# Kernel tuning notes

Hardware: AMD Instinct MI355X
Metric: run time of the kernel (lower is better)

## Reference

```python
import jax, jax.numpy as jnp
import numpy as np

E = 128       # embed_dim
H = 128       # hidden_dim
NLABEL = 5
VOCAB = 50000
DEPTH = 18    # levels 0..17, complete binary tree
BRANCH = 2
N_NODES = 2 ** DEPTH - 1  # level-order layout: level l occupies [2^l-1, 2^(l+1)-1)


def setup_inputs() -> dict:
    key = jax.random.key(0)
    ks = jax.random.split(key, 24)

    def w(k, shape):
        return jax.random.normal(k, shape, dtype=jnp.float32) * 0.05

    inp = {
        "embeds": w(ks[0], (VOCAB, E)),
        "node_words": jax.random.randint(ks[1], (N_NODES,), 0, VOCAB),
        "node_labels": jax.random.randint(ks[2], (N_NODES,), 0, NLABEL),
        "depth": DEPTH,
        "branching": BRANCH,
    }
    # 8 gate linears: *x maps E->H, *h maps H->H (torch nn.Linear: y = x @ W.T + b)
    for j, nm in enumerate(["ix", "ih", "fx", "fh", "ox", "oh", "ux", "uh"]):
        in_dim = E if nm.endswith("x") else H
        inp["W" + nm] = w(ks[3 + 2 * j], (H, in_dim))
        inp["b" + nm] = w(ks[4 + 2 * j], (H,))
    inp["Wout"] = w(ks[20], (NLABEL, H))
    inp["bout"] = w(ks[21], (NLABEL,))
    return inp


def _lin(x, W, b):
    return x @ W.T + b


def _tree_lstm(embeds, node_words, node_labels, depth, branching,
               Wix, bix, Wih, bih, Wfx, bfx, Wfh, bfh,
               Wox, box, Woh, boh, Wux, bux, Wuh, buh, Wout, bout):
    b = branching
    hid = Wix.shape[0]
    loss = jnp.zeros((), dtype=embeds.dtype)
    child_c = child_h = None
    logp = None
    # bottom-up over levels (leaves first); level l has b^l nodes at offset (b^l-1)/(b-1)
    for l in range(depth - 1, -1, -1):
        n = b ** l
        off = (b ** l - 1) // (b - 1)
        x = embeds[node_words[off:off + n]]            # [n, E]
        if child_h is None:                            # leaves: zero child states
            h_sum = jnp.zeros((n, hid), dtype=embeds.dtype)
            c_agg = jnp.zeros((n, hid), dtype=embeds.dtype)
        else:
            ch = child_h.reshape(n, b, hid)            # children of each level-l node
            cc = child_c.reshape(n, b, hid)
            h_sum = ch.sum(axis=1)                     # child-sum
            f = jax.nn.sigmoid(_lin(x, Wfx, bfx)[:, None, :] + _lin(ch, Wfh, bfh))
            c_agg = (f * cc).sum(axis=1)               # sum_k f_k * c_k
        i = jax.nn.sigmoid(_lin(x, Wix, bix) + _lin(h_sum, Wih, bih))
        o = jax.nn.sigmoid(_lin(x, Wox, box) + _lin(h_sum, Woh, boh))
        u = jnp.tanh(_lin(x, Wux, bux) + _lin(h_sum, Wuh, buh))
        c = i * u + c_agg
        h = o * jnp.tanh(c)
        logp = jax.nn.log_softmax(_lin(h, Wout, bout), axis=-1)   # [n, NLABEL]
        lab = node_labels[off:off + n]
        loss = loss - logp[jnp.arange(n), lab].sum()              # NLL summed over nodes
        child_c, child_h = c, h
    return logp, loss  # logp from level 0 = root log-probs [1, NLABEL]


def reference(embeds, node_words, node_labels, depth, branching,
              Wix, bix, Wih, bih, Wfx, bfx, Wfh, bfh,
              Wox, box, Woh, boh, Wux, bux, Wuh, buh, Wout, bout):
    return _tree_lstm(embeds, node_words, node_labels, depth, branching,
                      Wix, bix, Wih, bih, Wfx, bfx, Wfh, bfh,
                      Wox, box, Woh, boh, Wux, bux, Wuh, buh, Wout, bout)
```

## Files before the change

### kernel.cpp

```cpp
#include <hip/hip_runtime.h>
#include <math.h>

#define DEPTH 18
#define NINT ((1 << (DEPTH - 1)) - 1)
#define LEAF_OFF ((1 << (DEPTH - 2)) - 1)
#define NVOCAB 50000
#define SAW 520

typedef unsigned short bf16raw;
typedef __bf16 bf16x8 __attribute__((ext_vector_type(8)));
typedef float f32x4 __attribute__((ext_vector_type(4)));
typedef short short8 __attribute__((ext_vector_type(8)));

__device__ __forceinline__ float sigm(float x) { return 1.0f / (1.0f + __expf(-x)); }
__device__ __forceinline__ float fast_tanh(float x) {
    float t = __expf(2.0f * x);
    return 1.0f - 2.0f / (t + 1.0f);
}

__device__ __forceinline__ float bf2f(bf16raw u) {
    union { unsigned int i; float f; } v;
    v.i = ((unsigned int)u) << 16;
    return v.f;
}
__device__ __forceinline__ bf16raw f2bf(float f) {
    union { float f; unsigned int i; } v;
    v.f = f;
    unsigned int r = v.i + 0x7FFFu + ((v.i >> 16) & 1u);
    return (bf16raw)(r >> 16);
}

#define SB() __builtin_amdgcn_sched_barrier(0)

__global__ __launch_bounds__(256) void k_prep_embeds(const float* __restrict__ src,
                                                     bf16raw* __restrict__ dst, int n4)
{
    int i = blockIdx.x * blockDim.x + threadIdx.x;
    if (i < n4) {
        float4 v = ((const float4*)src)[i];
        ushort4 o;
        o.x = f2bf(v.x); o.y = f2bf(v.y); o.z = f2bf(v.z); o.w = f2bf(v.w);
        ((ushort4*)dst)[i] = o;
    }
}

__global__ __launch_bounds__(128) void k_prep_bcat(
    const float* __restrict__ Wix, const float* __restrict__ bix,
    const float* __restrict__ Wih, const float* __restrict__ bih,
    const float* __restrict__ Wfx, const float* __restrict__ bfx,
    const float* __restrict__ Wfh, const float* __restrict__ bfh,
    const float* __restrict__ Wox, const float* __restrict__ box_,
    const float* __restrict__ Woh, const float* __restrict__ boh,
    const float* __restrict__ Wux, const float* __restrict__ bux,
    const float* __restrict__ Wuh, const float* __restrict__ buh,
    bf16raw* __restrict__ Bfrag, float* __restrict__ bias_cat)
{
    const int j = blockIdx.x;
    const int gate = j >> 7, jj = j & 127;
    const float *Wx, *Wh, *bx, *bh;
    switch (gate) {
        case 0: Wx = Wix; Wh = Wih; bx = bix;  bh = bih; break;
        case 1: Wx = Wux; Wh = Wuh; bx = bux;  bh = buh; break;
        case 2: Wx = Wox; Wh = Woh; bx = box_; bh = boh; break;
        default: Wx = Wfx; Wh = Wfh; bx = bfx; bh = bfh; break;
    }
    const int coltile = (j >> 4) & 7, lr = j & 15;
    for (int k = threadIdx.x; k < 256; k += blockDim.x) {
        float v = (k < 128) ? Wx[jj * 128 + k] : Wh[jj * 128 + (k - 128)];
        const int idx = (((gate * 8 + coltile) * 8 + (k >> 5)) * 64
                         + ((k >> 3) & 3) * 16 + lr) * 8 + (k & 7);
        Bfrag[idx] = f2bf(v);
    }
    if (threadIdx.x == 0) bias_cat[j] = bx[jj] + bh[jj];
}

template<int CB>
__device__ __forceinline__ void lp_burst(const bf16raw* __restrict__ bfbase, int wcol,
                                         bf16x8 (&bb)[16])
{
#pragma unroll
    for (int kt = 0; kt < 4; ++kt)
#pragma unroll
        for (int j = 0; j < 4; ++j)
            bb[kt * 4 + j] = *(const bf16x8*)(bfbase +
                    (long)(((CB * 8 + (wcol >> 4) + j) * 8 + kt) * 512));
}

__device__ __forceinline__ void lp_mfma_all(const bf16raw* __restrict__ sA, int wrow,
                                            int lrow, int lquad,
                                            bf16x8 (&bb)[16], f32x4 (&acc)[4][4])
{
#pragma unroll
    for (int kt = 0; kt < 4; ++kt) {
        bf16x8 af[4];
#pragma unroll
        for (int i = 0; i < 4; ++i)
            af[i] = *(const bf16x8*)&sA[(wrow + i * 16 + lrow) * 136 + kt * 32 + lquad * 8];
#pragma unroll
        for (int i = 0; i < 4; ++i)
#pragma unroll
            for (int j = 0; j < 4; ++j)
                acc[i][j] = __builtin_amdgcn_mfma_f32_16x16x32_bf16(af[i], bb[kt * 4 + j], acc[i][j], 0, 0, 0);
    }
}

template<int CB>
__device__ __forceinline__ void lp_rungemm(const bf16raw* __restrict__ sA,
                                           const bf16raw* __restrict__ bfbase,
                                           int wrow, int wcol, int lrow, int lquad,
                                           f32x4 (&acc)[4][4])
{
#pragma unroll
    for (int i = 0; i < 4; i++)
#pragma unroll
        for (int j = 0; j < 4; j++) acc[i][j] = (f32x4){0.f, 0.f, 0.f, 0.f};
    bf16x8 bb[16];
    lp_burst<CB>(bfbase, wcol, bb);
    SB();
    lp_mfma_all(sA, wrow, lrow, lquad, bb, acc);
}

template<int G, int H>
__device__ __forceinline__ void load8(const bf16raw* __restrict__ bfbase, int w,
                                      bf16x8 (&bb)[8])
{
#pragma unroll
    for (int kt2 = 0; kt2 < 4; ++kt2)
#pragma unroll
        for (int jj = 0; jj < 2; ++jj)
            bb[kt2 * 2 + jj] = *(const bf16x8*)(bfbase +
                    (long)(((G * 8 + w * 2 + jj) * 8 + H * 4 + kt2) * 512));
}

template<int PASS, int H>
__device__ __forceinline__ void mfma8(const bf16raw* __restrict__ sA, int lrow, int lquad,
                                      bf16x8 (&bb)[8], f32x4 (&acc)[2][2])
{
    constexpr int base = (PASS == 2) ? (H ? 8 : 0)
                       : (PASS == 3) ? (H ? 12 : 0)
                       : H * 4;
#pragma unroll
    for (int kt2 = 0; kt2 < 4; ++kt2) {
        bf16x8 af[2];
#pragma unroll
        for (int i = 0; i < 2; ++i)
            af[i] = *(const bf16x8*)&sA[(i * 16 + lrow) * SAW + (base + kt2) * 32 + lquad * 8];
#pragma unroll
        for (int jj = 0; jj < 2; ++jj)
#pragma unroll
            for (int i = 0; i < 2; ++i)
                acc[i][jj] = __builtin_amdgcn_mfma_f32_16x16x32_bf16(af[i], bb[kt2 * 2 + jj], acc[i][jj], 0, 0, 0);
    }
}

__global__ __launch_bounds__(256, 2) void k_leafpre(
    const bf16raw* __restrict__ embeds_bf,
    const bf16raw* __restrict__ Bfrag, const float* __restrict__ bias_cat,
    const float* __restrict__ Wout, const float* __restrict__ bout,
    bf16raw* __restrict__ hc_leaf, float* __restrict__ lossv6, int vbase, int nv)
{
    vbase += blockIdx.x * 128;
    nv -= vbase;
    if (nv > 128) nv = 128;
    if (nv <= 0) return;

    __shared__ __align__(16) bf16raw sA[128 * 136];
    __shared__ __align__(16) bf16raw sT[128 * 136];
    __shared__ float sWout[5 * 128];

    const int t = threadIdx.x;
    for (int i = t; i < 640; i += 256) sWout[i] = Wout[i];

    {
        const int row = t >> 1;
        const int half = (t & 1) * 64;
        const int arow = (row < nv) ? row : 0;
        const bf16raw* ax = embeds_bf + (long)(vbase + arow) * 128;
#pragma unroll
        for (int s = 0; s < 8; ++s)
            *(short8*)&sA[row * 136 + half + s * 8] = *(const short8*)(ax + half + s * 8);
    }

    const int lane = t & 63;
    const int w = t >> 6;
    const int wrow = (w >> 1) * 64;
    const int wcol = (w & 1) * 64;
    const int lrow = lane & 15;
    const int lquad = lane >> 4;

    __syncthreads();

    const bf16raw* bfbase = Bfrag + (long)lane * 8;

    float tval[4][4][4];
    f32x4 acc[4][4];

    lp_rungemm<0>(sA, bfbase, wrow, wcol, lrow, lquad, acc);
#pragma unroll
    for (int i = 0; i < 4; i++)
#pragma unroll
        for (int jj = 0; jj < 4; jj++) {
            const float b = bias_cat[wcol + jj * 16 + lrow];
#pragma unroll
            for (int r = 0; r < 4; r++) tval[i][jj][r] = sigm(acc[i][jj][r] + b);
        }
    lp_rungemm<1>(sA, bfbase, wrow, wcol, lrow, lquad, acc);
#pragma unroll
    for (int i = 0; i < 4; i++)
#pragma unroll
        for (int jj = 0; jj < 4; jj++) {
            const float b = bias_cat[128 + wcol + jj * 16 + lrow];
#pragma unroll
            for (int r = 0; r < 4; r++) tval[i][jj][r] *= fast_tanh(acc[i][jj][r] + b);
        }
#pragma unroll
    for (int i = 0; i < 4; i++)
#pragma unroll
        for (int jj = 0; jj < 4; jj++)
#pragma unroll
            for (int r = 0; r < 4; r++) {
                const int m = wrow + i * 16 + lquad * 4 + r;
                const int j = wcol + jj * 16 + lrow;
                sT[m * 136 + j] = f2bf(tval[i][jj][r]);
            }
#pragma unroll
    for (int i = 0; i < 4; i++)
#pragma unroll
        for (int jj = 0; jj < 4; jj++)
#pragma unroll
            for (int r = 0; r < 4; r++) tval[i][jj][r] = fast_tanh(tval[i][jj][r]);
    __syncthreads();
#pragma unroll
    for (int s = 0; s < 8; ++s) {
        int ci = t + 256 * s;
        int row = ci >> 4, c8 = (ci & 15) * 8;
        if (row < nv)
            *(short8*)(hc_leaf + (long)(vbase + row) * 256 + 128 + c8) = *(const short8*)&sT[row * 136 + c8];
    }
    lp_rungemm<2>(sA, bfbase, wrow, wcol, lrow, lquad, acc);
    __syncthreads();
#pragma unroll
    for (int i = 0; i < 4; i++)
#pragma unroll
        for (int jj = 0; jj < 4; jj++) {
            const float b = bias_cat[256 + wcol + jj * 16 + lrow];
#pragma unroll
            for (int r = 0; r < 4; r++) {
                const int m = wrow + i * 16 + lquad * 4 + r;
                const int j = wcol + jj * 16 + lrow;
                sT[m * 136 + j] = f2bf(sigm(acc[i][jj][r] + b) * tval[i][jj][r]);
            }
        }
    __syncthreads();
#pragma unroll
    for (int s = 0; s < 8; ++s) {
        int ci = t + 256 * s;
        int row = ci >> 4, c8 = (ci & 15) * 8;
        if (row < nv)
            *(short8*)(hc_leaf + (long)(vbase + row) * 256 + c8) = *(const short8*)&sT[row * 136 + c8];
    }
    {
        const int row = t >> 1, half = t & 1;
        float p[5] = {0.f, 0.f, 0.f, 0.f, 0.f};
        const bf16raw* rp = &sT[row * 136 + half * 64];
#pragma unroll
        for (int s = 0; s < 8; ++s) {
            short8 v = *(const short8*)(rp + s * 8);
#pragma unroll
            for (int e = 0; e < 8; ++e) {
                float hv = bf2f((bf16raw)(unsigned short)v[e]);
#pragma unroll
                for (int l = 0; l < 5; l++) p[l] += hv * sWout[l * 128 + half * 64 + s * 8 + e];
            }
        }
#pragma unroll
        for (int l = 0; l < 5; l++) p[l] += __shfl_down(p[l], 1);
        if (half == 0 && row < nv) {
            float lg[5], mx = -1e30f;
#pragma unroll
            for (int l = 0; l < 5; l++) {
                lg[l] = p[l] + bout[l];
                mx = fmaxf(mx, lg[l]);
            }
            float se = 0.f;
#pragma unroll
            for (int l = 0; l < 5; l++) se += __expf(lg[l] - mx);
            float lse = __logf(se) + mx;
            float* dst = lossv6 + (long)(vbase + row) * 6;
#pragma unroll
            for (int l = 0; l < 5; l++) dst[l] = lg[l];
            dst[5] = lse;
        }
    }
}

__global__ __launch_bounds__(256, 3) void k_level32(
    const bf16raw* __restrict__ embeds_bf, const int* __restrict__ words,
    bf16raw* __restrict__ h_all, bf16raw* __restrict__ c_all,
    const bf16raw* __restrict__ hc_leaf,
    const bf16raw* __restrict__ Bfrag, const float* __restrict__ bias_cat,
    int off, int nm, int leafkids)
{
    __shared__ __align__(16) bf16raw sA[32 * SAW];
    __shared__ __align__(16) bf16raw sCT[64 * 136];

    const int t = threadIdx.x;
    const int m0 = blockIdx.x * 32;

    {
        const int row = t >> 3;
        const int co = (t & 7) * 8;
        int mm = m0 + row; if (mm >= nm) mm = nm - 1;
        const long g = (long)off + mm;
        const bf16raw* px = embeds_bf + (long)words[g] * 128;
        const bf16raw *p1, *p2;
        if (leafkids) {
            p1 = hc_leaf + (long)words[2 * g + 1] * 256;
            p2 = hc_leaf + (long)words[2 * g + 2] * 256;
        } else {
            p1 = h_all + (2 * g + 1) * 128;
            p2 = h_all + (2 * g + 2) * 128;
        }
        short8 vx0 = *(const short8*)(px + co);
        short8 vx1 = *(const short8*)(px + 64 + co);
        short8 h10 = *(const short8*)(p1 + co);
        short8 h11 = *(const short8*)(p1 + 64 + co);
        short8 h20 = *(const short8*)(p2 + co);
        short8 h21 = *(const short8*)(p2 + 64 + co);
        short8 hs0, hs1;
#pragma unroll
        for (int e = 0; e < 8; ++e) {
            hs0[e] = (short)f2bf(bf2f((bf16raw)(unsigned short)h10[e]) +
                                 bf2f((bf16raw)(unsigned short)h20[e]));
            hs1[e] = (short)f2bf(bf2f((bf16raw)(unsigned short)h11[e]) +
                                 bf2f((bf16raw)(unsigned short)h21[e]));
        }
        *(short8*)&sA[row * SAW + co]        = vx0;
        *(short8*)&sA[row * SAW + 64 + co]   = vx1;
        *(short8*)&sA[row * SAW + 128 + co]  = hs0;
        *(short8*)&sA[row * SAW + 192 + co]  = hs1;
        *(short8*)&sA[row * SAW + 256 + co]  = h10;
        *(short8*)&sA[row * SAW + 320 + co]  = h11;
        *(short8*)&sA[row * SAW + 384 + co]  = h20;
        *(short8*)&sA[row * SAW + 448 + co]  = h21;
    }
    {
        const int slot = t >> 2;
        const int cc8 = (t & 3) * 8;
        int mm = m0 + (slot >> 1); if (mm >= nm) mm = nm - 1;
        const long g = (long)off + mm;
        const long cg = 2 * g + 1 + (slot & 1);
        const bf16raw* pc = leafkids ? (hc_leaf + (long)words[cg] * 256 + 128)
                                     : (c_all + cg * 128);
#pragma unroll
        for (int s = 0; s < 4; ++s)
            *(short8*)&sCT[slot * 136 + s * 32 + cc8] = *(const short8*)(pc + s * 32 + cc8);
    }

    const int lane = t & 63;
    const int w = t >> 6;
    const int lrow = lane & 15;
    const int lquad = lane >> 4;

    float bias[4][2];
#pragma unroll
    for (int g = 0; g < 4; ++g)
#pragma unroll
        for (int jj = 0; jj < 2; ++jj)
            bias[g][jj] = bias_cat[g * 128 + w * 32 + jj * 16 + lrow];

    __syncthreads();

    const bf16raw* bfbase = Bfrag + (long)lane * 8;

    f32x4 acc[2][2];
    float si[2][2][4];
    float cc[2][2][4];
    float hh[2][2][4];
    bf16x8 bbA[8], bbB[8];

#define ZACC() { _Pragma("unroll") for (int i_ = 0; i_ < 2; ++i_) \
                 _Pragma("unroll") for (int j_ = 0; j_ < 2; ++j_) \
                     acc[i_][j_] = (f32x4){0.f, 0.f, 0.f, 0.f}; }

    load8<0, 0>(bfbase, w, bbA);
    load8<0, 1>(bfbase, w, bbB);
    SB();
    ZACC();
    mfma8<0, 0>(sA, lrow, lquad, bbA, acc); SB();
    load8<1, 0>(bfbase, w, bbA); SB();
    mfma8<0, 1>(sA, lrow, lquad, bbB, acc); SB();
    load8<1, 1>(bfbase, w, bbB); SB();
#pragma unroll
    for (int i = 0; i < 2; ++i)
#pragma unroll
        for (int jj = 0; jj < 2; ++jj)
#pragma unroll
            for (int r = 0; r < 4; ++r)
                si[i][jj][r] = sigm(acc[i][jj][r] + bias[0][jj]);
    ZACC();
    mfma8<1, 0>(sA, lrow, lquad, bbA, acc); SB();
    load8<3, 0>(bfbase, w, bbA); SB();
    mfma8<1, 1>(sA, lrow, lquad, bbB, acc); SB();
    load8<3, 1>(bfbase, w, bbB); SB();
#pragma unroll
    for (int i = 0; i < 2; ++i)
#pragma unroll
        for (int jj = 0; jj < 2; ++jj)
#pragma unroll
            for (int r = 0; r < 4; ++r)
                cc[i][jj][r] = si[i][jj][r] * fast_tanh(acc[i][jj][r] + bias[1][jj]);
    ZACC();
    mfma8<2, 0>(sA, lrow, lquad, bbA, acc);
    mfma8<2, 1>(sA, lrow, lquad, bbB, acc);
    SB();
#pragma unroll
    for (int i = 0; i < 2; ++i)
#pragma unroll
        for (int jj = 0; jj < 2; ++jj) {
            const int j = w * 32 + jj * 16 + lrow;
#pragma unroll
            for (int r = 0; r < 4; ++r) {
                const int m = i * 16 + lquad * 4 + r;
                cc[i][jj][r] += sigm(acc[i][jj][r] + bias[3][jj]) * bf2f(sCT[(2 * m) * 136 + j]);
            }
        }
    ZACC();
    mfma8<3, 0>(sA, lrow, lquad, bbA, acc);
    mfma8<3, 1>(sA, lrow, lquad, bbB, acc);
    SB();
    load8<2, 0>(bfbase, w, bbA);
    load8<2, 1>(bfbase, w, bbB);
    SB();
#pragma unroll
    for (int i = 0; i < 2; ++i)
#pragma unroll
        for (int jj = 0; jj < 2; ++jj) {
            const int j = w * 32 + jj * 16 + lrow;
#pragma unroll
            for (int r = 0; r < 4; ++r) {
                const int m = i * 16 + lquad * 4 + r;
                cc[i][jj][r] += sigm(acc[i][jj][r] + bias[3][jj]) * bf2f(sCT[(2 * m + 1) * 136 + j]);
            }
        }
    ZACC();
    mfma8<4, 0>(sA, lrow, lquad, bbA, acc);
    mfma8<4, 1>(sA, lrow, lquad, bbB, acc);
    SB();
#pragma unroll
    for (int i = 0; i < 2; ++i)
#pragma unroll
        for (int jj = 0; jj < 2; ++jj)
#pragma unroll
            for (int r = 0; r < 4; ++r)
                hh[i][jj][r] = sigm(acc[i][jj][r] + bias[2][jj]) * fast_tanh(cc[i][jj][r]);
#undef ZACC

    __syncthreads();

#pragma unroll
    for (int i = 0; i < 2; ++i)
#pragma unroll
        for (int jj = 0; jj < 2; ++jj) {
            const int j = w * 32 + jj * 16 + lrow;
#pragma unroll
            for (int r = 0; r < 4; ++r) {
                const int m = i * 16 + lquad * 4 + r;
                sCT[m * 136 + j] = f2bf(cc[i][jj][r]);
                sCT[(32 + m) * 136 + j] = f2bf(hh[i][jj][r]);
            }
        }
    __syncthreads();

#pragma unroll
    for (int q = 0; q < 4; ++q) {
        int ci = t + 256 * q;
        int row = ci >> 4;
        int c8 = (ci & 15) * 8;
        int m = row & 31;
        if (m0 + m < nm) {
            bf16raw* dst = (row < 32) ? c_all : h_all;
            *(short8*)(dst + ((long)off + m0 + m) * 128 + c8) = *(const short8*)&sCT[row * 136 + c8];
        }
    }
}

__global__ __launch_bounds__(256) void k_loss(
    const bf16raw* __restrict__ h_all, const int* __restrict__ words,
    const int* __restrict__ labels, const float* __restrict__ lossv6,
    const float* __restrict__ Wout, const float* __restrict__ bout,
    float* __restrict__ partials, float* __restrict__ out)
{
    __shared__ float sWout[640];
    __shared__ float red[128];
    const int t = threadIdx.x;
    for (int i = t; i < 640; i += 256) sWout[i] = Wout[i];

    const int row = t >> 1, half = t & 1;
    const long g = (long)blockIdx.x * 128 + row;
    const bool valid = g < NINT;
    const long gg = valid ? g : 0;
    __syncthreads();

    float p[5] = {0.f, 0.f, 0.f, 0.f, 0.f};
    const bf16raw* hp = h_all + gg * 128 + half * 64;
#pragma unroll
    for (int s = 0; s < 8; ++s) {
        short8 v = *(const short8*)(hp + s * 8);
#pragma unroll
        for (int e = 0; e < 8; ++e) {
            float hv = bf2f((bf16raw)(unsigned short)v[e]);
#pragma unroll
            for (int l = 0; l < 5; l++) p[l] += hv * sWout[l * 128 + half * 64 + s * 8 + e];
        }
    }
#pragma unroll
    for (int l = 0; l < 5; l++) p[l] += __shfl_down(p[l], 1);

    float lossNode = 0.f;
    if (half == 0 && valid) {
        float lg[5], mx = -1e30f;
#pragma unroll
        for (int l = 0; l < 5; l++) {
            lg[l] = p[l] + bout[l];
            mx = fmaxf(mx, lg[l]);
        }
        float se = 0.f;
#pragma unroll
        for (int l = 0; l < 5; l++) se += __expf(lg[l] - mx);
        float lse = __logf(se) + mx;
        lossNode = lse - lg[labels[gg]];
        if (gg >= LEAF_OFF) {
            const float* lv1 = lossv6 + (long)words[2 * gg + 1] * 6;
            const float* lv2 = lossv6 + (long)words[2 * gg + 2] * 6;
            lossNode += (lv1[5] - lv1[labels[2 * gg + 1]])
                      + (lv2[5] - lv2[labels[2 * gg + 2]]);
        }
        if (gg == 0) {
#pragma unroll
            for (int l = 0; l < 5; l++) out[l] = lg[l] - lse;
        }
    }
    if (half == 0) red[row] = lossNode;
    __syncthreads();
    if (t < 64) {
        float s = red[t] + red[t + 64];
#pragma unroll
        for (int d = 32; d > 0; d >>= 1) s += __shfl_down(s, d);
        if (t == 0) atomicAdd(&partials[blockIdx.x & 1023], s);
    }
}

__global__ __launch_bounds__(256) void k3_reduce(const float* __restrict__ partials,
                                                 float* __restrict__ out)
{
    const int t = threadIdx.x;
    float s = 0.f;
    for (int i = t; i < 1024; i += 256) s += partials[i];
#pragma unroll
    for (int d = 32; d > 0; d >>= 1) s += __shfl_down(s, d);
    __shared__ float red[4];
    if ((t & 63) == 0) red[t >> 6] = s;
    __syncthreads();
    if (t == 0) out[5] = red[0] + red[1] + red[2] + red[3];
}

extern "C" void kernel_launch(void* const* d_in, const int* in_sizes, int n_in,
                              void* d_out, int out_size, void* d_ws, size_t ws_size,
                              hipStream_t stream)
{
    const float* embeds = (const float*)d_in[0];
    const int* words = (const int*)d_in[1];
    const int* labels = (const int*)d_in[2];
    const float* Wix = (const float*)d_in[5],  *bix  = (const float*)d_in[6];
    const float* Wih = (const float*)d_in[7],  *bih  = (const float*)d_in[8];
    const float* Wfx = (const float*)d_in[9],  *bfx  = (const float*)d_in[10];
    const float* Wfh = (const float*)d_in[11], *bfh  = (const float*)d_in[12];
    const float* Wox = (const float*)d_in[13], *box_ = (const float*)d_in[14];
    const float* Woh = (const float*)d_in[15], *boh  = (const float*)d_in[16];
    const float* Wux = (const float*)d_in[17], *bux  = (const float*)d_in[18];
    const float* Wuh = (const float*)d_in[19], *buh  = (const float*)d_in[20];
    const float* Wout = (const float*)d_in[21], *bout = (const float*)d_in[22];
    float* out = (float*)d_out;

    char* ws = (char*)d_ws;
    const size_t treeElems = (size_t)NINT * 128;
    bf16raw* h_all = (bf16raw*)ws;
    bf16raw* c_all = h_all + treeElems;
    bf16raw* embeds_bf = c_all + treeElems;
    bf16raw* Bfrag = embeds_bf + (size_t)NVOCAB * 128;
    bf16raw* hc_leaf = Bfrag + 4 * 8 * 8 * 512;
    float* lossv6 = (float*)(hc_leaf + (size_t)NVOCAB * 256);
    float* bias_cat = lossv6 + (size_t)NVOCAB * 6;
    float* partials = bias_cat + 512;

    k_prep_embeds<<<(NVOCAB * 128 / 4 + 255) / 256, 256, 0, stream>>>(
        embeds, embeds_bf, NVOCAB * 128 / 4);
    k_prep_bcat<<<512, 128, 0, stream>>>(Wix, bix, Wih, bih, Wfx, bfx, Wfh, bfh,
                                         Wox, box_, Woh, boh, Wux, bux, Wuh, buh,
                                         Bfrag, bias_cat);
    hipMemsetAsync(partials, 0, 1024 * sizeof(float), stream);

    k_leafpre<<<(NVOCAB + 127) / 128, 256, 0, stream>>>(
        embeds_bf, Bfrag, bias_cat, Wout, bout, hc_leaf, lossv6, 0, NVOCAB);

    for (int l = DEPTH - 2; l >= 0; --l) {
        const int n = 1 << l;
        k_level32<<<dim3((n + 31) / 32), 256, 0, stream>>>(
            embeds_bf, words, h_all, c_all, hc_leaf, Bfrag, bias_cat,
            n - 1, n, (l == DEPTH - 2) ? 1 : 0);
    }

    k_loss<<<(NINT + 127) / 128, 256, 0, stream>>>(
        h_all, words, labels, lossv6, Wout, bout, partials, out);
    k3_reduce<<<1, 256, 0, stream>>>(partials, out);
}
```

Baseline: 378.0 us.

## Shrink leaf-precompute tiles to 64 rows and pad weight fragment stride

The vocabulary leaf-precompute kernel now handles 64 vocab rows per block instead of 128. Each wave covers 32x64 outputs, so the accumulator and activation registers are halved, LDS use drops, and launch bounds rise to 3 blocks per CU. The weight fragment layout is padded from 8 to 9 k-tiles per column tile, likely to spread global or cache access across channels. The trade-off is that every weight fragment is reloaded twice as often across blocks, and the output projection's LDS reads become scalar.

```diff
diff --git a/kernel.cpp b/kernel.cpp
--- a/kernel.cpp
+++ b/kernel.cpp
@@ -6,6 +6,7 @@
 #define LEAF_OFF ((1 << (DEPTH - 2)) - 1)
 #define NVOCAB 50000
 #define SAW 520
+#define KTS 9
 
 typedef unsigned short bf16raw;
 typedef __bf16 bf16x8 __attribute__((ext_vector_type(8)));
@@ -67,7 +68,7 @@
     const int coltile = (j >> 4) & 7, lr = j & 15;
     for (int k = threadIdx.x; k < 256; k += blockDim.x) {
         float v = (k < 128) ? Wx[jj * 128 + k] : Wh[jj * 128 + (k - 128)];
-        const int idx = (((gate * 8 + coltile) * 8 + (k >> 5)) * 64
+        const int idx = (((gate * 8 + coltile) * KTS + (k >> 5)) * 64
                          + ((k >> 3) & 3) * 16 + lr) * 8 + (k & 7);
         Bfrag[idx] = f2bf(v);
     }
@@ -83,21 +84,21 @@
 #pragma unroll
         for (int j = 0; j < 4; ++j)
             bb[kt * 4 + j] = *(const bf16x8*)(bfbase +
-                    (long)(((CB * 8 + (wcol >> 4) + j) * 8 + kt) * 512));
+                    (long)(((CB * 8 + (wcol >> 4) + j) * KTS + kt) * 512));
 }
 
 __device__ __forceinline__ void lp_mfma_all(const bf16raw* __restrict__ sA, int wrow,
                                             int lrow, int lquad,
-                                            bf16x8 (&bb)[16], f32x4 (&acc)[4][4])
+                                            bf16x8 (&bb)[16], f32x4 (&acc)[2][4])
 {
 #pragma unroll
     for (int kt = 0; kt < 4; ++kt) {
-        bf16x8 af[4];
-#pragma unroll
-        for (int i = 0; i < 4; ++i)
+        bf16x8 af[2];
+#pragma unroll
+        for (int i = 0; i < 2; ++i)
             af[i] = *(const bf16x8*)&sA[(wrow + i * 16 + lrow) * 136 + kt * 32 + lquad * 8];
 #pragma unroll
-        for (int i = 0; i < 4; ++i)
+        for (int i = 0; i < 2; ++i)
 #pragma unroll
             for (int j = 0; j < 4; ++j)
                 acc[i][j] = __builtin_amdgcn_mfma_f32_16x16x32_bf16(af[i], bb[kt * 4 + j], acc[i][j], 0, 0, 0);
@@ -108,10 +109,10 @@
 __device__ __forceinline__ void lp_rungemm(const bf16raw* __restrict__ sA,
                                            const bf16raw* __restrict__ bfbase,
                                            int wrow, int wcol, int lrow, int lquad,
-                                           f32x4 (&acc)[4][4])
-{
-#pragma unroll
-    for (int i = 0; i < 4; i++)
+                                           f32x4 (&acc)[2][4])
+{
+#pragma unroll
+    for (int i = 0; i < 2; i++)
 #pragma unroll
         for (int j = 0; j < 4; j++) acc[i][j] = (f32x4){0.f, 0.f, 0.f, 0.f};
     bf16x8 bb[16];
@@ -129,7 +130,7 @@
 #pragma unroll
         for (int jj = 0; jj < 2; ++jj)
             bb[kt2 * 2 + jj] = *(const bf16x8*)(bfbase +
-                    (long)(((G * 8 + w * 2 + jj) * 8 + H * 4 + kt2) * 512));
+                    (long)(((G * 8 + w * 2 + jj) * KTS + H * 4 + kt2) * 512));
 }
 
 template<int PASS, int H>
@@ -153,38 +154,39 @@
     }
 }
 
-__global__ __launch_bounds__(256, 2) void k_leafpre(
+__global__ __launch_bounds__(256, 3) void k_leafpre(
     const bf16raw* __restrict__ embeds_bf,
     const bf16raw* __restrict__ Bfrag, const float* __restrict__ bias_cat,
     const float* __restrict__ Wout, const float* __restrict__ bout,
-    bf16raw* __restrict__ hc_leaf, float* __restrict__ lossv6, int vbase, int nv)
-{
-    vbase += blockIdx.x * 128;
-    nv -= vbase;
-    if (nv > 128) nv = 128;
+    bf16raw* __restrict__ hc_leaf, float* __restrict__ lossv6, int nvtot)
+{
+    const int vbase = blockIdx.x * 64;
+    int nv = nvtot - vbase;
+    if (nv > 64) nv = 64;
     if (nv <= 0) return;
 
-    __shared__ __align__(16) bf16raw sA[128 * 136];
-    __shared__ __align__(16) bf16raw sT[128 * 136];
+    __shared__ __align__(16) bf16raw sA[64 * 136];
+    __shared__ __align__(16) bf16raw sT[64 * 136];
     __shared__ float sWout[5 * 128];
 
     const int t = threadIdx.x;
     for (int i = t; i < 640; i += 256) sWout[i] = Wout[i];
 
     {
-        const int row = t >> 1;
-        const int half = (t & 1) * 64;
+        const int row = t >> 2;
+        const int co = (t & 3) * 32;
         const int arow = (row < nv) ? row : 0;
         const bf16raw* ax = embeds_bf + (long)(vbase + arow) * 128;
-#pragma unroll
-        for (int s = 0; s < 8; ++s)
-            *(short8*)&sA[row * 136 + half + s * 8] = *(const short8*)(ax + half + s * 8);
+        *(short8*)&sA[row * 136 + co]      = *(const short8*)(ax + co);
+        *(short8*)&sA[row * 136 + co + 8]  = *(const short8*)(ax + co + 8);
+        *(short8*)&sA[row * 136 + co + 16] = *(const short8*)(ax + co + 16);
+        *(short8*)&sA[row * 136 + co + 24] = *(const short8*)(ax + co + 24);
     }
 
     const int lane = t & 63;
     const int w = t >> 6;
-    const int wrow = (w >> 1) * 64;
-    const int wcol = (w & 1) * 64;
+    const int wrow = (w & 1) * 32;
+    const int wcol = (w >> 1) * 64;
     const int lrow = lane & 15;
     const int lquad = lane >> 4;
 
@@ -192,12 +194,12 @@
 
     const bf16raw* bfbase = Bfrag + (long)lane * 8;
 
-    float tval[4][4][4];
-    f32x4 acc[4][4];
+    float tval[2][4][4];
+    f32x4 acc[2][4];
 
     lp_rungemm<0>(sA, bfbase, wrow, wcol, lrow, lquad, acc);
 #pragma unroll
-    for (int i = 0; i < 4; i++)
+    for (int i = 0; i < 2; i++)
 #pragma unroll
         for (int jj = 0; jj < 4; jj++) {
             const float b = bias_cat[wcol + jj * 16 + lrow];
@@ -206,7 +208,7 @@
         }
     lp_rungemm<1>(sA, bfbase, wrow, wcol, lrow, lquad, acc);
 #pragma unroll
-    for (int i = 0; i < 4; i++)
+    for (int i = 0; i < 2; i++)
 #pragma unroll
         for (int jj = 0; jj < 4; jj++) {
             const float b = bias_cat[128 + wcol + jj * 16 + lrow];
@@ -214,7 +216,7 @@
             for (int r = 0; r < 4; r++) tval[i][jj][r] *= fast_tanh(acc[i][jj][r] + b);
         }
 #pragma unroll
-    for (int i = 0; i < 4; i++)
+    for (int i = 0; i < 2; i++)
 #pragma unroll
         for (int jj = 0; jj < 4; jj++)
 #pragma unroll
@@ -224,14 +226,14 @@
                 sT[m * 136 + j] = f2bf(tval[i][jj][r]);
             }
 #pragma unroll
-    for (int i = 0; i < 4; i++)
+    for (int i = 0; i < 2; i++)
 #pragma unroll
         for (int jj = 0; jj < 4; jj++)
 #pragma unroll
             for (int r = 0; r < 4; r++) tval[i][jj][r] = fast_tanh(tval[i][jj][r]);
     __syncthreads();
 #pragma unroll
-    for (int s = 0; s < 8; ++s) {
+    for (int s = 0; s < 4; ++s) {
         int ci = t + 256 * s;
         int row = ci >> 4, c8 = (ci & 15) * 8;
         if (row < nv)
@@ -240,7 +242,7 @@
     lp_rungemm<2>(sA, bfbase, wrow, wcol, lrow, lquad, acc);
     __syncthreads();
 #pragma unroll
-    for (int i = 0; i < 4; i++)
+    for (int i = 0; i < 2; i++)
 #pragma unroll
         for (int jj = 0; jj < 4; jj++) {
             const float b = bias_cat[256 + wcol + jj * 16 + lrow];
@@ -253,29 +255,27 @@
         }
     __syncthreads();
 #pragma unroll
-    for (int s = 0; s < 8; ++s) {
+    for (int s = 0; s < 4; ++s) {
         int ci = t + 256 * s;
         int row = ci >> 4, c8 = (ci & 15) * 8;
         if (row < nv)
             *(short8*)(hc_leaf + (long)(vbase + row) * 256 + c8) = *(const short8*)&sT[row * 136 + c8];
     }
     {
-        const int row = t >> 1, half = t & 1;
+        const int row = t >> 2, q = t & 3;
         float p[5] = {0.f, 0.f, 0.f, 0.f, 0.f};
-        const bf16raw* rp = &sT[row * 136 + half * 64];
-#pragma unroll
-        for (int s = 0; s < 8; ++s) {
-            short8 v = *(const short8*)(rp + s * 8);
-#pragma unroll
-            for (int e = 0; e < 8; ++e) {
-                float hv = bf2f((bf16raw)(unsigned short)v[e]);
-#pragma unroll
-                for (int l = 0; l < 5; l++) p[l] += hv * sWout[l * 128 + half * 64 + s * 8 + e];
-            }
-        }
-#pragma unroll
-        for (int l = 0; l < 5; l++) p[l] += __shfl_down(p[l], 1);
-        if (half == 0 && row < nv) {
+        for (int k0 = 0; k0 < 32; ++k0) {
+            const int k = q * 32 + k0;
+            float hv = bf2f(sT[row * 136 + k]);
+#pragma unroll
+            for (int l = 0; l < 5; l++) p[l] += hv * sWout[l * 128 + k];
+        }
+#pragma unroll
+        for (int l = 0; l < 5; l++) {
+            p[l] += __shfl_down(p[l], 2);
+            p[l] += __shfl_down(p[l], 1);
+        }
+        if (q == 0 && row < nv) {
             float lg[5], mx = -1e30f;
 #pragma unroll
             for (int l = 0; l < 5; l++) {
@@ -589,7 +589,7 @@
     bf16raw* c_all = h_all + treeElems;
     bf16raw* embeds_bf = c_all + treeElems;
     bf16raw* Bfrag = embeds_bf + (size_t)NVOCAB * 128;
-    bf16raw* hc_leaf = Bfrag + 4 * 8 * 8 * 512;
+    bf16raw* hc_leaf = Bfrag + 4 * 8 * KTS * 512;
     float* lossv6 = (float*)(hc_leaf + (size_t)NVOCAB * 256);
     float* bias_cat = lossv6 + (size_t)NVOCAB * 6;
     float* partials = bias_cat + 512;
@@ -601,8 +601,8 @@
                                          Bfrag, bias_cat);
     hipMemsetAsync(partials, 0, 1024 * sizeof(float), stream);
 
-    k_leafpre<<<(NVOCAB + 127) / 128, 256, 0, stream>>>(
-        embeds_bf, Bfrag, bias_cat, Wout, bout, hc_leaf, lossv6, 0, NVOCAB);
+    k_leafpre<<<(NVOCAB + 63) / 64, 256, 0, stream>>>(
+        embeds_bf, Bfrag, bias_cat, Wout, bout, hc_leaf, lossv6, NVOCAB);
 
     for (int l = DEPTH - 2; l >= 0; --l) {
         const int n = 1 << l;
```

Measured after the change: 372.2 us. No clear change (-1.5%).
